# Kernel optimization log

Measured on AMD Instinct MI355X. Metric: run time of the kernel, lower is better.

## Reference

```python
import jax, jax.numpy as jnp
import numpy as np

EPS = 1e-5
NB, NP, NA, NROT = 16, 1024, 12, 60
C0, C1 = 64, 128
CIN, CFEAT, COUT = 256, 512, 256


def _bn(x, g, b):
    # training-mode BatchNorm1d: stats over batch (+ spatial) dims, channel dim 1
    axes = (0,) if x.ndim == 2 else (0, 2)
    m = x.mean(axis=axes, keepdims=True)
    v = x.var(axis=axes, keepdims=True)
    sh = [1] * x.ndim; sh[1] = -1
    return (x - m) * jax.lax.rsqrt(v + EPS) * g.reshape(sh) + b.reshape(sh)


def _hat(v):  # (n,3) -> (n,3,3) skew-symmetric
    z = jnp.zeros_like(v[:, 0])
    return jnp.stack([z, -v[:, 2], v[:, 1],
                      v[:, 2], z, -v[:, 0],
                      -v[:, 1], v[:, 0], z], axis=-1).reshape(-1, 3, 3)


def _exp_so3(v):  # Rodrigues formula, (n,3) -> (n,3,3)
    theta = jnp.linalg.norm(v, axis=-1, keepdims=True)  # (n,1)
    k = v / jnp.where(theta < 1e-8, 1.0, theta)
    K = _hat(k)
    s = jnp.sin(theta)[..., None]
    c = (1.0 - jnp.cos(theta))[..., None]
    I = jnp.eye(3, dtype=v.dtype)
    return I + s * K + c * (K @ K)


def _pointnet(xyz, feats, W, b, g, bb):
    # PointnetSO3Conv: concat xyz (expanded over anchors) with feats, 1x1 conv, max over points
    nb, _, npts, na = feats.shape
    x = jnp.concatenate([jnp.broadcast_to(xyz[:, :, :, None], (nb, 3, npts, na)), feats], axis=1)
    y = jnp.einsum('oc,bcpa->bopa', W, x) + b[None, :, None, None]
    y = y.max(axis=2)  # max over points -> (nb, o, na)
    return jax.nn.relu(_bn(y, g, bb))


def setup_inputs() -> dict:
    key = jax.random.key(0)
    ks = iter(jax.random.split(key, 64))
    def nrm(shape, s=0.1):
        return jax.random.normal(next(ks), shape, dtype=jnp.float32) * s
    d = {
        'xyz0': nrm((NB, 3, NP), 1.0),
        'feats0': nrm((NB, C0, NP, NA), 1.0),
        'xyz1': nrm((NB, 3, NP), 1.0),
        'feats1': nrm((NB, C1, NP, NA), 1.0),
        'trace_idx': jax.random.randint(next(ks), (NA, NROT), 0, NA),
        'anchors': nrm((NROT, 3, 3), 1.0),
        'pn0_W': nrm((C0, C0 + 3)), 'pn0_b': nrm((C0,)), 'pn0_g': jnp.ones((C0,), jnp.float32), 'pn0_bb': jnp.zeros((C0,), jnp.float32),
        'pn1_W': nrm((C1, C1 + 3)), 'pn1_b': nrm((C1,)), 'pn1_g': jnp.ones((C1,), jnp.float32), 'pn1_bb': jnp.zeros((C1,), jnp.float32),
        'lin_W': nrm((CIN, C0 + C1)), 'lin_b': nrm((CIN,)), 'lin_g': jnp.ones((CIN,), jnp.float32), 'lin_bb': jnp.zeros((CIN,), jnp.float32),
        'feat_W': nrm((CFEAT, CIN * NA)), 'feat_b': nrm((CFEAT,)), 'feat_g': jnp.ones((CFEAT,), jnp.float32), 'feat_bb': jnp.zeros((CFEAT,), jnp.float32),
        'att_W1': nrm((128, CFEAT)), 'att_b1': nrm((128,)), 'att_g': jnp.ones((128,), jnp.float32), 'att_bb': jnp.zeros((128,), jnp.float32),
        'att_W2': nrm((1, 128)), 'att_b2': nrm((1,)),
        'reg_W1': nrm((128, CFEAT)), 'reg_b1': nrm((128,)), 'reg_g': jnp.ones((128,), jnp.float32), 'reg_bb': jnp.zeros((128,), jnp.float32),
        'reg_W2': nrm((7, 128)), 'reg_b2': nrm((7,)),
        'out_W1': nrm((CFEAT, CFEAT)), 'out_b1': nrm((CFEAT,)), 'out_g': jnp.ones((CFEAT,), jnp.float32), 'out_bb': jnp.zeros((CFEAT,), jnp.float32),
        'out_W2': nrm((COUT, CFEAT)), 'out_b2': nrm((COUT,)),
    }
    return d


def reference(xyz0, feats0, xyz1, feats1, trace_idx, anchors,
              pn0_W, pn0_b, pn0_g, pn0_bb, pn1_W, pn1_b, pn1_g, pn1_bb,
              lin_W, lin_b, lin_g, lin_bb, feat_W, feat_b, feat_g, feat_bb,
              att_W1, att_b1, att_g, att_bb, att_W2, att_b2,
              reg_W1, reg_b1, reg_g, reg_bb, reg_W2, reg_b2,
              out_W1, out_b1, out_g, out_bb, out_W2, out_b2):
    nb = feats0.shape[0]
    # _pooling: per-level pointnet + BN + relu, concat, pn_linear + pn_bn
    p0 = _pointnet(xyz0, feats0, pn0_W, pn0_b, pn0_g, pn0_bb)
    p1 = _pointnet(xyz1, feats1, pn1_W, pn1_b, pn1_g, pn1_bb)
    x = jnp.concatenate([p0, p1], axis=1)                                   # (nb, 192, na)
    x = _bn(jnp.einsum('oc,bca->boa', lin_W, x) + lin_b[None, :, None], lin_g, lin_bb)  # (nb,256,na)
    # gather trace_idx_ori and flatten channel x anchor dims
    x = x[:, :, trace_idx].reshape(nb, CIN * NA, NROT)                      # (nb,3072,60)
    xf = jax.nn.relu(_bn(jnp.einsum('oc,bca->boa', feat_W, x) + feat_b[None, :, None], feat_g, feat_bb))  # (nb,512,60)
    h = jax.nn.relu(_bn(jnp.einsum('oc,bca->boa', reg_W1, xf) + reg_b1[None, :, None], reg_g, reg_bb))
    residual = (jnp.einsum('oc,bca->boa', reg_W2, h) + reg_b2[None, :, None]).transpose(0, 2, 1)  # (nb,60,7)
    res_D = residual[:, :, :3] / jnp.linalg.norm(residual[:, :, :3], axis=-1, keepdims=True)
    res_N = (jax.nn.sigmoid(residual[:, :, 3]) - 0.5) * jnp.pi / 5
    res_V = res_D * res_N[..., None]
    res_R = _exp_so3(res_V.reshape(-1, 3)).reshape(nb, NROT, 3, 3)
    res_T = residual[:, :, 4:]
    pred_R = jnp.einsum('tij,btjk->btik', anchors, res_R)
    # attention head + softmax over 60 rotations
    a = jax.nn.relu(_bn(jnp.einsum('oc,bca->boa', att_W1, xf) + att_b1[None, :, None], att_g, att_bb))
    logits = (jnp.einsum('oc,bca->boa', att_W2, a) + att_b2[None, :, None])[:, 0]   # (nb,60)
    x_attn = jax.nn.softmax(logits, axis=-1)
    # max-pool over rotations + out MLP
    xm = xf.max(axis=-1)                                                    # (nb,512)
    o = jax.nn.relu(_bn(xm @ out_W1.T + out_b1, out_g, out_bb))
    x_out = o @ out_W2.T + out_b2
    return (x_out, x_attn, pred_R, res_T)
```

## Files before the change

### kernel.cpp

```cpp
#include <hip/hip_runtime.h>
#include <math.h>

#define NBATCH 16
#define NPTS   1024
#define NANG   12
#define NROTS  60
#define EPSV   1e-5f

#define WB0_OFF   0
#define WB1_OFF   3072
#define PART0_OFF 13312
#define PART1_OFF 799744
#define FEATW_OFF 13312
#define XF_OFF    13312
#define XM_OFF    504832
#define OACT_OFF  513024
#define XCAT_OFF  2372608
#define XLIN_OFF  2409472
#define XG_OFF    2458624
#define BRP_OFF   2458624
#define HACT_OFF  4424704
#define AACT_OFF  4547584
#define FRAW_OFF  5407744

#define OUT_XOUT 0
#define OUT_ATTN 4096
#define OUT_PRED 5056
#define OUT_REST 13696

typedef short  bf16x8 __attribute__((ext_vector_type(8)));
typedef float  f32x4  __attribute__((ext_vector_type(4)));

__device__ __forceinline__ unsigned short f2bf_rne(float x){
  unsigned int u = __float_as_uint(x);
  u += 0x7FFFu + ((u >> 16) & 1u);
  return (unsigned short)(u >> 16);
}
__device__ __forceinline__ float bf2f(unsigned short h){
  return __uint_as_float(((unsigned int)h) << 16);
}

__device__ __forceinline__ bf16x8 pack8(const float* f){
  union { unsigned int u[4]; bf16x8 v; } r;
  #pragma unroll
  for (int i = 0; i < 4; i++)
    r.u[i] = __builtin_amdgcn_perm(__float_as_uint(f[2*i+1]),
                                   __float_as_uint(f[2*i]), 0x07060302u);
  return r.v;
}

__device__ __forceinline__ void stage16(const unsigned short* g, unsigned short* l){
  __builtin_amdgcn_global_load_lds((const __attribute__((address_space(1))) void*)g,
                                   (__attribute__((address_space(3))) void*)l, 16, 0, 0);
}

template<int NT>
__device__ __forceinline__ void block_stats(float v, float& m, float& var, float* sbuf){
  constexpr int NW = NT / 64;
  float s = v, s2 = v * v;
  #pragma unroll
  for (int off = 32; off; off >>= 1){
    s  += __shfl_xor(s,  off, 64);
    s2 += __shfl_xor(s2, off, 64);
  }
  const int w = threadIdx.x >> 6;
  if ((threadIdx.x & 63) == 0){ sbuf[w] = s; sbuf[NW + w] = s2; }
  __syncthreads();
  float ts = 0.f, ts2 = 0.f;
  #pragma unroll
  for (int i = 0; i < NW; i++){ ts += sbuf[i]; ts2 += sbuf[NW + i]; }
  m = ts / (float)NT;
  var = ts2 / (float)NT - m * m;
}

template<int C>
__global__ void prep_wb(const float* __restrict__ W, unsigned short* __restrict__ Wb){
  constexpr int KPAD = C + 32;
  const int idx = blockIdx.x * 256 + threadIdx.x;
  if (idx >= C * KPAD) return;
  const int o = idx / KPAD, k = idx % KPAD;
  float v = 0.f;
  if (k < C)          v = W[(size_t)o * (C + 3) + 3 + k];
  else if (k < C + 3) v = W[(size_t)o * (C + 3) + (k - C)];
  Wb[idx] = f2bf_rne(v);
}

template<int C>
__global__ __launch_bounds__(256) void pn_mfma(
    const float* __restrict__ xyz, const float* __restrict__ feats,
    const unsigned short* __restrict__ Wb, float* __restrict__ part){
  constexpr int KPAD = C + 32;
  constexpr int NFK  = C / 32;
  constexpr int MT   = C / 16;
  constexpr int SROW = 196;
  const int nchunk = blockIdx.x, b = blockIdx.y;
  const int tid  = threadIdx.x;
  const int lane = tid & 63, wave = tid >> 6;
  const int g = lane >> 4, l16 = lane & 15;
  const int colbase = wave * 48;
  const int nbase   = nchunk * 192;

  __shared__ float Bs[2][32 * SROW];

  int nn[3], pp[3];
  #pragma unroll
  for (int t = 0; t < 3; t++){
    nn[t] = colbase + t * 16 + l16;
    pp[t] = (nbase + nn[t]) / 12;
  }

  f32x4 acc[MT][3];
  #pragma unroll
  for (int m = 0; m < MT; m++)
    #pragma unroll
    for (int t = 0; t < 3; t++)
      acc[m][t] = (f32x4){0.f, 0.f, 0.f, 0.f};

  const float* fB = feats + (size_t)b * C * (NPTS * NANG) + nbase;

  int srow[6], scol[6], sslot[6];
  #pragma unroll
  for (int jj = 0; jj < 6; jj++){
    const int idx = tid + 256 * jj;
    srow[jj]  = idx / 48;
    scol[jj]  = (idx % 48) * 4;
    sslot[jj] = (srow[jj] & 7) * 4 + (srow[jj] >> 3);
  }

  {
    float4 v[6];
    #pragma unroll
    for (int jj = 0; jj < 6; jj++)
      v[jj] = *(const float4*)(fB + (size_t)srow[jj] * (NPTS * NANG) + scol[jj]);
    #pragma unroll
    for (int jj = 0; jj < 6; jj++)
      *(float4*)(&Bs[0][sslot[jj] * SROW + scol[jj]]) = v[jj];
  }
  __syncthreads();

  #pragma unroll
  for (int ks = 0; ks < NFK; ks++){
    const int buf = ks & 1;
    float4 v[6];
    if (ks + 1 < NFK){
      const int kb = (ks + 1) * 32;
      #pragma unroll
      for (int jj = 0; jj < 6; jj++)
        v[jj] = *(const float4*)(fB + (size_t)(kb + srow[jj]) * (NPTS * NANG) + scol[jj]);
    }
    const int kb = ks * 32;
    bf16x8 Bf[3];
    #pragma unroll
    for (int t = 0; t < 3; t++){
      float f[8];
      #pragma unroll
      for (int j = 0; j < 8; j++)
        f[j] = Bs[buf][(j * 4 + g) * SROW + nn[t]];
      Bf[t] = pack8(f);
    }
    #pragma unroll
    for (int m = 0; m < MT; m++){
      const bf16x8 Af = *(const bf16x8*)(Wb + (size_t)(m * 16 + l16) * KPAD + kb + g * 8);
      #pragma unroll
      for (int t = 0; t < 3; t++)
        acc[m][t] = __builtin_amdgcn_mfma_f32_16x16x32_bf16(Af, Bf[t], acc[m][t], 0, 0, 0);
    }
    if (ks + 1 < NFK){
      #pragma unroll
      for (int jj = 0; jj < 6; jj++)
        *(float4*)(&Bs[buf ^ 1][sslot[jj] * SROW + scol[jj]]) = v[jj];
    }
    __syncthreads();
  }

  {
    const int kb = C;
    bf16x8 Bf[3];
    #pragma unroll
    for (int t = 0; t < 3; t++){
      float f[8];
      #pragma unroll
      for (int j = 0; j < 8; j++) f[j] = 0.f;
      if (g == 0){
        #pragma unroll
        for (int j = 0; j < 3; j++)
          f[j] = xyz[(size_t)(b * 3 + j) * NPTS + pp[t]];
      }
      Bf[t] = pack8(f);
    }
    #pragma unroll
    for (int m = 0; m < MT; m++){
      const bf16x8 Af = *(const bf16x8*)(Wb + (size_t)(m * 16 + l16) * KPAD + kb + g * 8);
      #pragma unroll
      for (int t = 0; t < 3; t++)
        acc[m][t] = __builtin_amdgcn_mfma_f32_16x16x32_bf16(Af, Bf[t], acc[m][t], 0, 0, 0);
    }
  }

  float* yb = &Bs[0][0];
  #pragma unroll
  for (int m = 0; m < MT; m++){
    __syncthreads();
    #pragma unroll
    for (int t = 0; t < 3; t++)
      #pragma unroll
      for (int r = 0; r < 4; r++)
        yb[(g * 4 + r) * SROW + nn[t]] = acc[m][t][r];
    __syncthreads();
    if (tid < 192){
      const int o_l = tid / 12, a = tid % 12;
      float mx = -3.4e38f;
      #pragma unroll
      for (int pl = 0; pl < 16; pl++)
        mx = fmaxf(mx, yb[o_l * SROW + pl * 12 + a]);
      part[((size_t)(b * 64 + nchunk) * C + m * 16 + o_l) * 12 + a] = mx;
    }
  }
}

__global__ void pn_reduce_bn(const float* __restrict__ part0, const float* __restrict__ part1,
    const float* __restrict__ b0, const float* __restrict__ g0, const float* __restrict__ bb0,
    const float* __restrict__ b1, const float* __restrict__ g1, const float* __restrict__ bb1,
    float* __restrict__ xcat){
  const int ch = blockIdx.x, t = threadIdx.x;
  const int b = t / 12, a = t % 12;
  const float* part; const float *bias, *g, *bb; int o, Cl;
  if (ch < 64){ part = part0; bias = b0; g = g0; bb = bb0; o = ch;      Cl = 64;  }
  else        { part = part1; bias = b1; g = g1; bb = bb1; o = ch - 64; Cl = 128; }
  const float* pp = part + ((size_t)(b * 64) * Cl + o) * 12 + a;
  const size_t kstride = (size_t)Cl * 12;
  float v = pp[0];
  for (int k = 1; k < 64; k++) v = fmaxf(v, pp[(size_t)k * kstride]);
  v += bias[o];
  __shared__ float sbuf[8];
  float m, var;
  block_stats<192>(v, m, var, sbuf);
  float xn = (v - m) * rsqrtf(var + EPSV) * g[o] + bb[o];
  xcat[((size_t)b * 192 + ch) * 12 + a] = fmaxf(xn, 0.f);
}

__global__ void lin_bn(const float* __restrict__ xcat, const float* __restrict__ W,
    const float* __restrict__ bias, const float* __restrict__ g, const float* __restrict__ bb,
    float* __restrict__ xlin){
  const int o = blockIdx.x, t = threadIdx.x;
  const int b = t / 12, a = t % 12;
  const float* xr = xcat + (size_t)b * 2304 + a;
  const float* wr = W + (size_t)o * 192;
  float v = bias[o];
  for (int c = 0; c < 192; c++) v = fmaf(wr[c], xr[(size_t)c * 12], v);
  __shared__ float sbuf[8];
  float m, var;
  block_stats<192>(v, m, var, sbuf);
  xlin[((size_t)b * 256 + o) * 12 + a] = (v - m) * rsqrtf(var + EPSV) * g[o] + bb[o];
}

__global__ void prep_featw(const float* __restrict__ W, unsigned short* __restrict__ Wb2){
  const int idx = blockIdx.x * 256 + threadIdx.x;
  if (idx >= 512 * 3072) return;
  const int o = idx / 3072, k = idx % 3072;
  const float x = W[idx];
  const unsigned short hi = f2bf_rne(x);
  const unsigned short lo = f2bf_rne(x - bf2f(hi));
  Wb2[(size_t)o * 6144 + k] = hi;
  Wb2[(size_t)o * 6144 + 3072 + k] = lo;
}

__global__ void prep_xg(const float* __restrict__ xlin, const int* __restrict__ trace,
                        unsigned short* __restrict__ Xg){
  const int n = blockIdx.x;
  const int b = n / 60, r = n % 60;
  unsigned short* row = Xg + (size_t)n * 6144;
  __shared__ int ta[12];
  if (threadIdx.x < 12) ta[threadIdx.x] = trace[threadIdx.x * 60 + r];
  __syncthreads();
  for (int i = threadIdx.x; i < 3072; i += 256){
    const int c = i / 12, a = i % 12;
    const float x = xlin[((size_t)b * 256 + c) * 12 + ta[a]];
    const unsigned short hi = f2bf_rne(x);
    const unsigned short lo = f2bf_rne(x - bf2f(hi));
    row[i] = hi;
    row[3072 + i] = lo;
  }
}

__global__ __launch_bounds__(256) void feat_mfma(
    const unsigned short* __restrict__ Wb2, const unsigned short* __restrict__ Xg,
    float* __restrict__ fraw){
  const int nblk = blockIdx.x, mblk = blockIdx.y, seg = blockIdx.z;
  const int tid = threadIdx.x;
  const int lane = tid & 63, wave = tid >> 6;
  const int g = lane >> 4, l16 = lane & 15;
  const int kA = (seg == 1) ? 3072 : 0;
  const int kB = (seg == 2) ? 3072 : 0;
  const int sw = l16 & 7;
  const int wm = wave >> 1, wn = wave & 1;

  __shared__ unsigned short As[2][64 * 64];
  __shared__ unsigned short Bs[2][64 * 64];

  int rowj[2], colj[2], ldsoff[2];
  #pragma unroll
  for (int j = 0; j < 2; j++){
    const int idx = j * 256 + wave * 64 + lane;
    rowj[j]   = idx >> 3;
    colj[j]   = ((idx & 7) ^ (rowj[j] & 7)) * 8;
    ldsoff[j] = (j * 256 + wave * 64) * 8;
  }
  const unsigned short* Agb = Wb2 + (size_t)mblk * 64 * 6144 + kA;
  const unsigned short* Bgb = Xg  + (size_t)nblk * 64 * 6144 + kB;

  f32x4 acc[2][2];
  #pragma unroll
  for (int i = 0; i < 2; i++)
    #pragma unroll
    for (int j = 0; j < 2; j++)
      acc[i][j] = (f32x4){0.f, 0.f, 0.f, 0.f};

  #pragma unroll
  for (int j = 0; j < 2; j++){
    stage16(Agb + (size_t)rowj[j] * 6144 + colj[j], &As[0][ldsoff[j]]);
    stage16(Bgb + (size_t)rowj[j] * 6144 + colj[j], &Bs[0][ldsoff[j]]);
  }
  __syncthreads();

  for (int kc = 0; kc < 3072; kc += 64){
    const int buf = (kc >> 6) & 1;
    if (kc + 64 < 3072){
      const int kn = kc + 64;
      #pragma unroll
      for (int j = 0; j < 2; j++){
        stage16(Agb + (size_t)rowj[j] * 6144 + kn + colj[j], &As[buf ^ 1][ldsoff[j]]);
        stage16(Bgb + (size_t)rowj[j] * 6144 + kn + colj[j], &Bs[buf ^ 1][ldsoff[j]]);
      }
    }
    #pragma unroll
    for (int kc2 = 0; kc2 < 64; kc2 += 32){
      const int c0 = kc2 >> 3;
      bf16x8 af[2], bfr[2];
      #pragma unroll
      for (int i = 0; i < 2; i++)
        af[i]  = *(const bf16x8*)&As[buf][(wm * 32 + i * 16 + l16) * 64 + ((c0 + g) ^ sw) * 8];
      #pragma unroll
      for (int i = 0; i < 2; i++)
        bfr[i] = *(const bf16x8*)&Bs[buf][(wn * 32 + i * 16 + l16) * 64 + ((c0 + g) ^ sw) * 8];
      #pragma unroll
      for (int i = 0; i < 2; i++)
        #pragma unroll
        for (int j = 0; j < 2; j++)
          acc[i][j] = __builtin_amdgcn_mfma_f32_16x16x32_bf16(af[i], bfr[j], acc[i][j], 0, 0, 0);
    }
    __syncthreads();
  }

  float* base = fraw + (size_t)seg * (512 * 960);
  #pragma unroll
  for (int i = 0; i < 2; i++)
    #pragma unroll
    for (int j = 0; j < 2; j++){
      const int n = nblk * 64 + wn * 32 + j * 16 + l16;
      #pragma unroll
      for (int q = 0; q < 4; q++){
        const int m = mblk * 64 + wm * 32 + i * 16 + g * 4 + q;
        base[(size_t)m * 960 + n] = acc[i][j][q];
      }
    }
}

__global__ void feat_bn(const float* __restrict__ fraw, const float* __restrict__ bias,
    const float* __restrict__ g, const float* __restrict__ bb,
    float* __restrict__ xf, float* __restrict__ xm){
  const int o = blockIdx.x, t = threadIdx.x;
  const int b = t / 60, r = t % 60;
  const size_t SS = (size_t)512 * 960;
  const size_t in = (size_t)o * 960 + t;
  float v = fraw[in] + fraw[SS + in] + fraw[2 * SS + in] + bias[o];
  __shared__ float sbuf[32];
  float m, var;
  block_stats<960>(v, m, var, sbuf);
  const float xn = fmaxf((v - m) * rsqrtf(var + EPSV) * g[o] + bb[o], 0.f);
  xf[((size_t)b * 512 + o) * 60 + r] = xn;
  __shared__ float red[960];
  red[t] = xn;
  __syncthreads();
  if (r == 0){
    float mx = red[t];
    for (int k = 1; k < 60; k++) mx = fmaxf(mx, red[t + k]);
    xm[(size_t)b * 512 + o] = mx;
  }
}

__global__ __launch_bounds__(256) void brgemm2(const float* __restrict__ xf,
    const float* __restrict__ Wr, const float* __restrict__ Wa,
    float* __restrict__ brp){
  const int og = blockIdx.x, b = blockIdx.y, z = blockIdx.z;
  const int br = z >> 3, ks = z & 7;
  const float* W = br ? Wa : Wr;
  const int lane = threadIdx.x & 63, wave = threadIdx.x >> 6;
  const int obase = og * 32 + wave * 8;
  const int rr = lane < 60 ? lane : 0;
  const float* xb = xf + ((size_t)b * 512 + ks * 64) * 60 + rr;
  const float* wr = W + (size_t)obase * 512 + ks * 64;

  float acc[8];
  #pragma unroll
  for (int i = 0; i < 8; i++) acc[i] = 0.f;

  float cur[4], nxt[4];
  #pragma unroll
  for (int j = 0; j < 4; j++) cur[j] = xb[(size_t)j * 60];

  for (int c0 = 0; c0 < 64; c0 += 4){
    #pragma unroll
    for (int j = 0; j < 4; j++){
      int cc = c0 + 4 + j; if (cc > 63) cc = 63;
      nxt[j] = xb[(size_t)cc * 60];
    }
    #pragma unroll
    for (int j = 0; j < 4; j++)
      #pragma unroll
      for (int i = 0; i < 8; i++)
        acc[i] = fmaf(wr[(size_t)i * 512 + c0 + j], cur[j], acc[i]);
    #pragma unroll
    for (int j = 0; j < 4; j++) cur[j] = nxt[j];
  }

  if (lane < 60){
    #pragma unroll
    for (int i = 0; i < 8; i++)
      brp[(((size_t)z * NBATCH + b) * 128 + obase + i) * 60 + lane] = acc[i];
  }
}

__global__ void br_bn(const float* __restrict__ brp,
    const float* __restrict__ biasR, const float* __restrict__ gR, const float* __restrict__ bbR,
    const float* __restrict__ biasA, const float* __restrict__ gA, const float* __restrict__ bbA,
    float* __restrict__ hact, float* __restrict__ aact){
  const int o = blockIdx.x, br = blockIdx.y, t = threadIdx.x;
  const int b = t / 60, r = t % 60;
  const float* bias = br ? biasA : biasR;
  const float* g    = br ? gA    : gR;
  const float* bb   = br ? bbA   : bbR;
  float v = bias[o];
  #pragma unroll
  for (int ks = 0; ks < 8; ks++)
    v += brp[((((size_t)br * 8 + ks) * NBATCH + b) * 128 + o) * 60 + r];
  __shared__ float sbuf[32];
  float m, var;
  block_stats<960>(v, m, var, sbuf);
  float* outp = br ? aact : hact;
  outp[((size_t)b * 128 + o) * 60 + r] =
      fmaxf((v - m) * rsqrtf(var + EPSV) * g[o] + bb[o], 0.f);
}

__global__ void reg2_geom(const float* __restrict__ h, const float* __restrict__ W2,
    const float* __restrict__ b2, const float* __restrict__ anchors, float* __restrict__ out){
  const int b = blockIdx.x, lane = threadIdx.x;
  const int r = lane < 60 ? lane : 59;
  float res[7];
  #pragma unroll
  for (int j = 0; j < 7; j++){
    float acc = b2[j];
    for (int c = 0; c < 128; c++)
      acc = fmaf(W2[j * 128 + c], h[((size_t)b * 128 + c) * 60 + r], acc);
    res[j] = acc;
  }
  if (lane >= 60) return;
  const float n = sqrtf(res[0]*res[0] + res[1]*res[1] + res[2]*res[2]);
  const float invn = 1.f / n;
  const float Nv = (1.f / (1.f + expf(-res[3])) - 0.5f) * 3.14159265358979323846f / 5.f;
  const float v0 = res[0]*invn*Nv, v1 = res[1]*invn*Nv, v2 = res[2]*invn*Nv;
  const float th = sqrtf(v0*v0 + v1*v1 + v2*v2);
  const float invt = th < 1e-8f ? 1.f : 1.f / th;
  const float k0 = v0*invt, k1 = v1*invt, k2 = v2*invt;
  const float s = sinf(th), cc = 1.f - cosf(th);
  const float K[9] = {0.f, -k2, k1,  k2, 0.f, -k0,  -k1, k0, 0.f};
  float K2[9];
  #pragma unroll
  for (int ii = 0; ii < 3; ii++)
    #pragma unroll
    for (int jj = 0; jj < 3; jj++)
      K2[ii*3+jj] = K[ii*3+0]*K[0*3+jj] + K[ii*3+1]*K[1*3+jj] + K[ii*3+2]*K[2*3+jj];
  float R[9];
  #pragma unroll
  for (int ii = 0; ii < 3; ii++)
    #pragma unroll
    for (int jj = 0; jj < 3; jj++)
      R[ii*3+jj] = (ii == jj ? 1.f : 0.f) + s * K[ii*3+jj] + cc * K2[ii*3+jj];
  const float* A = anchors + (size_t)r * 9;
  #pragma unroll
  for (int ii = 0; ii < 3; ii++)
    #pragma unroll
    for (int kk = 0; kk < 3; kk++){
      const float pv = A[ii*3+0]*R[0*3+kk] + A[ii*3+1]*R[1*3+kk] + A[ii*3+2]*R[2*3+kk];
      out[OUT_PRED + ((size_t)b * 60 + r) * 9 + ii * 3 + kk] = pv;
    }
  #pragma unroll
  for (int k = 0; k < 3; k++)
    out[OUT_REST + ((size_t)b * 60 + r) * 3 + k] = res[4 + k];
}

__global__ void att2_softmax(const float* __restrict__ a, const float* __restrict__ W2,
    const float* __restrict__ b2, float* __restrict__ out){
  const int b = blockIdx.x, lane = threadIdx.x;
  const int r = lane < 60 ? lane : 59;
  float acc = b2[0];
  for (int c = 0; c < 128; c++)
    acc = fmaf(W2[c], a[((size_t)b * 128 + c) * 60 + r], acc);
  const float l = lane < 60 ? acc : -INFINITY;
  float mx = l;
  #pragma unroll
  for (int off = 32; off; off >>= 1) mx = fmaxf(mx, __shfl_xor(mx, off, 64));
  const float e = lane < 60 ? expf(l - mx) : 0.f;
  float ssum = e;
  #pragma unroll
  for (int off = 32; off; off >>= 1) ssum += __shfl_xor(ssum, off, 64);
  if (lane < 60) out[OUT_ATTN + (size_t)b * 60 + lane] = e / ssum;
}

__global__ void out_head1(const float* __restrict__ xm, const float* __restrict__ W1,
    const float* __restrict__ b1, const float* __restrict__ g, const float* __restrict__ bb,
    float* __restrict__ o_act){
  const int t = threadIdx.x;
  const int b = t & 15, j = t >> 4;
  const int oc = blockIdx.x * 8 + j;
  float acc = b1[oc];
  const float* wr = W1 + (size_t)oc * 512;
  const float* xr = xm + (size_t)b * 512;
  for (int c = 0; c < 512; c++) acc = fmaf(wr[c], xr[c], acc);
  float s = acc, s2 = acc * acc;
  #pragma unroll
  for (int off = 8; off; off >>= 1){
    s  += __shfl_xor(s,  off, 16);
    s2 += __shfl_xor(s2, off, 16);
  }
  const float m = s * (1.f / 16.f);
  const float var = s2 * (1.f / 16.f) - m * m;
  o_act[(size_t)b * 512 + oc] = fmaxf((acc - m) * rsqrtf(var + EPSV) * g[oc] + bb[oc], 0.f);
}

__global__ void out_head2(const float* __restrict__ o_act, const float* __restrict__ W2,
    const float* __restrict__ b2, float* __restrict__ out){
  const int b = blockIdx.x, j = threadIdx.x;
  const float* wr = W2 + (size_t)j * 512;
  const float* xr = o_act + (size_t)b * 512;
  float acc = b2[j];
  for (int c = 0; c < 512; c++) acc = fmaf(wr[c], xr[c], acc);
  out[OUT_XOUT + (size_t)b * 256 + j] = acc;
}

extern "C" void kernel_launch(void* const* d_in, const int* in_sizes, int n_in,
                              void* d_out, int out_size, void* d_ws, size_t ws_size,
                              hipStream_t stream){
  const float* xyz0    = (const float*)d_in[0];
  const float* feats0  = (const float*)d_in[1];
  const float* xyz1    = (const float*)d_in[2];
  const float* feats1  = (const float*)d_in[3];
  const int*   trace   = (const int*)  d_in[4];
  const float* anchors = (const float*)d_in[5];
  const float* pn0_W  = (const float*)d_in[6];
  const float* pn0_b  = (const float*)d_in[7];
  const float* pn0_g  = (const float*)d_in[8];
  const float* pn0_bb = (const float*)d_in[9];
  const float* pn1_W  = (const float*)d_in[10];
  const float* pn1_b  = (const float*)d_in[11];
  const float* pn1_g  = (const float*)d_in[12];
  const float* pn1_bb = (const float*)d_in[13];
  const float* lin_W  = (const float*)d_in[14];
  const float* lin_b  = (const float*)d_in[15];
  const float* lin_g  = (const float*)d_in[16];
  const float* lin_bb = (const float*)d_in[17];
  const float* feat_W  = (const float*)d_in[18];
  const float* feat_b  = (const float*)d_in[19];
  const float* feat_g  = (const float*)d_in[20];
  const float* feat_bb = (const float*)d_in[21];
  const float* att_W1 = (const float*)d_in[22];
  const float* att_b1 = (const float*)d_in[23];
  const float* att_g  = (const float*)d_in[24];
  const float* att_bb = (const float*)d_in[25];
  const float* att_W2 = (const float*)d_in[26];
  const float* att_b2 = (const float*)d_in[27];
  const float* reg_W1 = (const float*)d_in[28];
  const float* reg_b1 = (const float*)d_in[29];
  const float* reg_g  = (const float*)d_in[30];
  const float* reg_bb = (const float*)d_in[31];
  const float* reg_W2 = (const float*)d_in[32];
  const float* reg_b2 = (const float*)d_in[33];
  const float* out_W1 = (const float*)d_in[34];
  const float* out_b1 = (const float*)d_in[35];
  const float* out_g  = (const float*)d_in[36];
  const float* out_bb = (const float*)d_in[37];
  const float* out_W2 = (const float*)d_in[38];
  const float* out_b2 = (const float*)d_in[39];

  float* ws  = (float*)d_ws;
  float* out = (float*)d_out;
  unsigned short* wb0 = (unsigned short*)(ws + WB0_OFF);
  unsigned short* wb1 = (unsigned short*)(ws + WB1_OFF);
  unsigned short* fw  = (unsigned short*)(ws + FEATW_OFF);
  unsigned short* xg  = (unsigned short*)(ws + XG_OFF);

  prep_wb<64> <<<24, 256, 0, stream>>>(pn0_W, wb0);
  prep_wb<128><<<80, 256, 0, stream>>>(pn1_W, wb1);

  pn_mfma<64> <<<dim3(64, 16), 256, 0, stream>>>(xyz0, feats0, wb0, ws + PART0_OFF);
  pn_mfma<128><<<dim3(64, 16), 256, 0, stream>>>(xyz1, feats1, wb1, ws + PART1_OFF);

  pn_reduce_bn<<<192, 192, 0, stream>>>(ws + PART0_OFF, ws + PART1_OFF,
      pn0_b, pn0_g, pn0_bb, pn1_b, pn1_g, pn1_bb, ws + XCAT_OFF);

  prep_featw<<<6144, 256, 0, stream>>>(feat_W, fw);

  lin_bn<<<256, 192, 0, stream>>>(ws + XCAT_OFF, lin_W, lin_b, lin_g, lin_bb, ws + XLIN_OFF);

  prep_xg<<<960, 256, 0, stream>>>(ws + XLIN_OFF, trace, xg);

  feat_mfma<<<dim3(15, 8, 3), 256, 0, stream>>>(fw, xg, ws + FRAW_OFF);
  feat_bn<<<512, 960, 0, stream>>>(ws + FRAW_OFF, feat_b, feat_g, feat_bb,
                                   ws + XF_OFF, ws + XM_OFF);

  brgemm2<<<dim3(4, 16, 16), 256, 0, stream>>>(ws + XF_OFF, reg_W1, att_W1, ws + BRP_OFF);
  br_bn<<<dim3(128, 2), 960, 0, stream>>>(ws + BRP_OFF,
      reg_b1, reg_g, reg_bb, att_b1, att_g, att_bb,
      ws + HACT_OFF, ws + AACT_OFF);

  reg2_geom<<<16, 64, 0, stream>>>(ws + HACT_OFF, reg_W2, reg_b2, anchors, out);
  att2_softmax<<<16, 64, 0, stream>>>(ws + AACT_OFF, att_W2, att_b2, out);
  out_head1<<<64, 128, 0, stream>>>(ws + XM_OFF, out_W1, out_b1, out_g, out_bb, ws + OACT_OFF);
  out_head2<<<16, 256, 0, stream>>>(ws + OACT_OFF, out_W2, out_b2, out);
}
```

Before: 485.9 us.

## Merge independent kernels to cut launch count and run pointnet branches concurrently

Result: faster. 431.1 us (-11.3%).

```diff
diff --git a/kernel.cpp b/kernel.cpp
--- a/kernel.cpp
+++ b/kernel.cpp
@@ -11,7 +11,6 @@
 #define WB1_OFF   3072
 #define PART0_OFF 13312
 #define PART1_OFF 799744
-#define FEATW_OFF 13312
 #define XF_OFF    13312
 #define XM_OFF    504832
 #define OACT_OFF  513024
@@ -22,6 +21,7 @@
 #define HACT_OFF  4424704
 #define AACT_OFF  4547584
 #define FRAW_OFF  5407744
+#define FEATW_OFF 6882304
 
 #define OUT_XOUT 0
 #define OUT_ATTN 4096
@@ -74,9 +74,9 @@
 }
 
 template<int C>
-__global__ void prep_wb(const float* __restrict__ W, unsigned short* __restrict__ Wb){
+__device__ __forceinline__ void prep_wb_body(int idx, const float* __restrict__ W,
+                                             unsigned short* __restrict__ Wb){
   constexpr int KPAD = C + 32;
-  const int idx = blockIdx.x * 256 + threadIdx.x;
   if (idx >= C * KPAD) return;
   const int o = idx / KPAD, k = idx % KPAD;
   float v = 0.f;
@@ -85,14 +85,36 @@
   Wb[idx] = f2bf_rne(v);
 }
 
+__global__ __launch_bounds__(256) void prep_all(
+    const float* __restrict__ W0, const float* __restrict__ W1,
+    const float* __restrict__ FW,
+    unsigned short* __restrict__ wb0, unsigned short* __restrict__ wb1,
+    unsigned short* __restrict__ fw2){
+  const int blk = blockIdx.x;
+  if (blk < 24){
+    prep_wb_body<64>(blk * 256 + threadIdx.x, W0, wb0);
+  } else if (blk < 104){
+    prep_wb_body<128>((blk - 24) * 256 + threadIdx.x, W1, wb1);
+  } else {
+    const int idx = (blk - 104) * 256 + threadIdx.x;
+    const int o = idx / 3072, k = idx % 3072;
+    const float x = FW[idx];
+    const unsigned short hi = f2bf_rne(x);
+    const unsigned short lo = f2bf_rne(x - bf2f(hi));
+    fw2[(size_t)o * 6144 + k] = hi;
+    fw2[(size_t)o * 6144 + 3072 + k] = lo;
+  }
+}
+
+#define SROW 196
 template<int C>
-__global__ __launch_bounds__(256) void pn_mfma(
+__device__ __forceinline__ void pn_body(
     const float* __restrict__ xyz, const float* __restrict__ feats,
-    const unsigned short* __restrict__ Wb, float* __restrict__ part){
+    const unsigned short* __restrict__ Wb, float* __restrict__ part,
+    float* Bs ){
   constexpr int KPAD = C + 32;
   constexpr int NFK  = C / 32;
   constexpr int MT   = C / 16;
-  constexpr int SROW = 196;
   const int nchunk = blockIdx.x, b = blockIdx.y;
   const int tid  = threadIdx.x;
   const int lane = tid & 63, wave = tid >> 6;
@@ -100,8 +122,6 @@
   const int colbase = wave * 48;
   const int nbase   = nchunk * 192;
 
-  __shared__ float Bs[2][32 * SROW];
-
   int nn[3], pp[3];
   #pragma unroll
   for (int t = 0; t < 3; t++){
@@ -134,13 +154,14 @@
       v[jj] = *(const float4*)(fB + (size_t)srow[jj] * (NPTS * NANG) + scol[jj]);
     #pragma unroll
     for (int jj = 0; jj < 6; jj++)
-      *(float4*)(&Bs[0][sslot[jj] * SROW + scol[jj]]) = v[jj];
+      *(float4*)(&Bs[sslot[jj] * SROW + scol[jj]]) = v[jj];
   }
   __syncthreads();
 
   #pragma unroll
   for (int ks = 0; ks < NFK; ks++){
-    const int buf = ks & 1;
+    float* Bc = Bs + (ks & 1) * (32 * SROW);
+    float* Bn = Bs + ((ks & 1) ^ 1) * (32 * SROW);
     float4 v[6];
     if (ks + 1 < NFK){
       const int kb = (ks + 1) * 32;
@@ -155,7 +176,7 @@
       float f[8];
       #pragma unroll
       for (int j = 0; j < 8; j++)
-        f[j] = Bs[buf][(j * 4 + g) * SROW + nn[t]];
+        f[j] = Bc[(j * 4 + g) * SROW + nn[t]];
       Bf[t] = pack8(f);
     }
     #pragma unroll
@@ -168,7 +189,7 @@
     if (ks + 1 < NFK){
       #pragma unroll
       for (int jj = 0; jj < 6; jj++)
-        *(float4*)(&Bs[buf ^ 1][sslot[jj] * SROW + scol[jj]]) = v[jj];
+        *(float4*)(&Bn[sslot[jj] * SROW + scol[jj]]) = v[jj];
     }
     __syncthreads();
   }
@@ -197,7 +218,7 @@
     }
   }
 
-  float* yb = &Bs[0][0];
+  float* yb = Bs;
   #pragma unroll
   for (int m = 0; m < MT; m++){
     __syncthreads();
@@ -216,6 +237,16 @@
       part[((size_t)(b * 64 + nchunk) * C + m * 16 + o_l) * 12 + a] = mx;
     }
   }
+}
+
+__global__ __launch_bounds__(256) void pn_both(
+    const float* __restrict__ xyz0, const float* __restrict__ feats0,
+    const unsigned short* __restrict__ wb0, float* __restrict__ part0,
+    const float* __restrict__ xyz1, const float* __restrict__ feats1,
+    const unsigned short* __restrict__ wb1, float* __restrict__ part1){
+  __shared__ float Bs[2 * 32 * SROW];
+  if (blockIdx.z == 0) pn_body<64> (xyz0, feats0, wb0, part0, Bs);
+  else                 pn_body<128>(xyz1, feats1, wb1, part1, Bs);
 }
 
 __global__ void pn_reduce_bn(const float* __restrict__ part0, const float* __restrict__ part1,
@@ -252,17 +283,6 @@
   float m, var;
   block_stats<192>(v, m, var, sbuf);
   xlin[((size_t)b * 256 + o) * 12 + a] = (v - m) * rsqrtf(var + EPSV) * g[o] + bb[o];
-}
-
-__global__ void prep_featw(const float* __restrict__ W, unsigned short* __restrict__ Wb2){
-  const int idx = blockIdx.x * 256 + threadIdx.x;
-  if (idx >= 512 * 3072) return;
-  const int o = idx / 3072, k = idx % 3072;
-  const float x = W[idx];
-  const unsigned short hi = f2bf_rne(x);
-  const unsigned short lo = f2bf_rne(x - bf2f(hi));
-  Wb2[(size_t)o * 6144 + k] = hi;
-  Wb2[(size_t)o * 6144 + 3072 + k] = lo;
 }
 
 __global__ void prep_xg(const float* __restrict__ xlin, const int* __restrict__ trace,
@@ -389,14 +409,39 @@
   }
 }
 
-__global__ __launch_bounds__(256) void brgemm2(const float* __restrict__ xf,
+__global__ __launch_bounds__(256) void brgemm_oh1(const float* __restrict__ xf,
     const float* __restrict__ Wr, const float* __restrict__ Wa,
-    float* __restrict__ brp){
-  const int og = blockIdx.x, b = blockIdx.y, z = blockIdx.z;
+    float* __restrict__ brp,
+    const float* __restrict__ xm, const float* __restrict__ oW1,
+    const float* __restrict__ ob1, const float* __restrict__ og,
+    const float* __restrict__ obb, float* __restrict__ o_act){
+  const int z = blockIdx.z;
+  if (z == 16){
+    const int q = blockIdx.y * 4 + blockIdx.x;
+    if (q >= 32) return;
+    const int t = threadIdx.x;
+    const int b = t & 15, j = t >> 4;
+    const int oc = q * 16 + j;
+    float acc = ob1[oc];
+    const float* wr = oW1 + (size_t)oc * 512;
+    const float* xr = xm + (size_t)b * 512;
+    for (int c = 0; c < 512; c++) acc = fmaf(wr[c], xr[c], acc);
+    float s = acc, s2 = acc * acc;
+    #pragma unroll
+    for (int off = 8; off; off >>= 1){
+      s  += __shfl_xor(s,  off, 16);
+      s2 += __shfl_xor(s2, off, 16);
+    }
+    const float m = s * (1.f / 16.f);
+    const float var = s2 * (1.f / 16.f) - m * m;
+    o_act[(size_t)b * 512 + oc] = fmaxf((acc - m) * rsqrtf(var + EPSV) * og[oc] + obb[oc], 0.f);
+    return;
+  }
+  const int og_ = blockIdx.x, b = blockIdx.y;
   const int br = z >> 3, ks = z & 7;
   const float* W = br ? Wa : Wr;
   const int lane = threadIdx.x & 63, wave = threadIdx.x >> 6;
-  const int obase = og * 32 + wave * 8;
+  const int obase = og_ * 32 + wave * 8;
   const int rr = lane < 60 ? lane : 0;
   const float* xb = xf + ((size_t)b * 512 + ks * 64) * 60 + rr;
   const float* wr = W + (size_t)obase * 512 + ks * 64;
@@ -452,100 +497,79 @@
       fmaxf((v - m) * rsqrtf(var + EPSV) * g[o] + bb[o], 0.f);
 }
 
-__global__ void reg2_geom(const float* __restrict__ h, const float* __restrict__ W2,
-    const float* __restrict__ b2, const float* __restrict__ anchors, float* __restrict__ out){
-  const int b = blockIdx.x, lane = threadIdx.x;
-  const int r = lane < 60 ? lane : 59;
-  float res[7];
-  #pragma unroll
-  for (int j = 0; j < 7; j++){
-    float acc = b2[j];
+__global__ void heads(
+    const float* __restrict__ h, const float* __restrict__ rW2,
+    const float* __restrict__ rb2, const float* __restrict__ anchors,
+    const float* __restrict__ a, const float* __restrict__ aW2, const float* __restrict__ ab2,
+    const float* __restrict__ o_act, const float* __restrict__ oW2,
+    const float* __restrict__ ob2, float* __restrict__ out){
+  const int b = blockIdx.x, sel = blockIdx.y, t = threadIdx.x;
+  if (sel == 0){
+    if (t >= 64) return;
+    const int r = t < 60 ? t : 59;
+    float res[7];
+    #pragma unroll
+    for (int j = 0; j < 7; j++) res[j] = rb2[j];
+    for (int c = 0; c < 128; c++){
+      const float hv = h[((size_t)b * 128 + c) * 60 + r];
+      #pragma unroll
+      for (int j = 0; j < 7; j++) res[j] = fmaf(rW2[j * 128 + c], hv, res[j]);
+    }
+    if (t >= 60) return;
+    const float n = sqrtf(res[0]*res[0] + res[1]*res[1] + res[2]*res[2]);
+    const float invn = 1.f / n;
+    const float Nv = (1.f / (1.f + expf(-res[3])) - 0.5f) * 3.14159265358979323846f / 5.f;
+    const float v0 = res[0]*invn*Nv, v1 = res[1]*invn*Nv, v2 = res[2]*invn*Nv;
+    const float th = sqrtf(v0*v0 + v1*v1 + v2*v2);
+    const float invt = th < 1e-8f ? 1.f : 1.f / th;
+    const float k0 = v0*invt, k1 = v1*invt, k2 = v2*invt;
+    const float s = sinf(th), cc = 1.f - cosf(th);
+    const float K[9] = {0.f, -k2, k1,  k2, 0.f, -k0,  -k1, k0, 0.f};
+    float K2[9];
+    #pragma unroll
+    for (int ii = 0; ii < 3; ii++)
+      #pragma unroll
+      for (int jj = 0; jj < 3; jj++)
+        K2[ii*3+jj] = K[ii*3+0]*K[0*3+jj] + K[ii*3+1]*K[1*3+jj] + K[ii*3+2]*K[2*3+jj];
+    float R[9];
+    #pragma unroll
+    for (int ii = 0; ii < 3; ii++)
+      #pragma unroll
+      for (int jj = 0; jj < 3; jj++)
+        R[ii*3+jj] = (ii == jj ? 1.f : 0.f) + s * K[ii*3+jj] + cc * K2[ii*3+jj];
+    const float* A = anchors + (size_t)t * 9;
+    #pragma unroll
+    for (int ii = 0; ii < 3; ii++)
+      #pragma unroll
+      for (int kk = 0; kk < 3; kk++){
+        const float pv = A[ii*3+0]*R[0*3+kk] + A[ii*3+1]*R[1*3+kk] + A[ii*3+2]*R[2*3+kk];
+        out[OUT_PRED + ((size_t)b * 60 + t) * 9 + ii * 3 + kk] = pv;
+      }
+    #pragma unroll
+    for (int k = 0; k < 3; k++)
+      out[OUT_REST + ((size_t)b * 60 + t) * 3 + k] = res[4 + k];
+  } else if (sel == 1){
+    if (t >= 64) return;
+    const int r = t < 60 ? t : 59;
+    float acc = ab2[0];
     for (int c = 0; c < 128; c++)
-      acc = fmaf(W2[j * 128 + c], h[((size_t)b * 128 + c) * 60 + r], acc);
-    res[j] = acc;
-  }
-  if (lane >= 60) return;
-  const float n = sqrtf(res[0]*res[0] + res[1]*res[1] + res[2]*res[2]);
-  const float invn = 1.f / n;
-  const float Nv = (1.f / (1.f + expf(-res[3])) - 0.5f) * 3.14159265358979323846f / 5.f;
-  const float v0 = res[0]*invn*Nv, v1 = res[1]*invn*Nv, v2 = res[2]*invn*Nv;
-  const float th = sqrtf(v0*v0 + v1*v1 + v2*v2);
-  const float invt = th < 1e-8f ? 1.f : 1.f / th;
-  const float k0 = v0*invt, k1 = v1*invt, k2 = v2*invt;
-  const float s = sinf(th), cc = 1.f - cosf(th);
-  const float K[9] = {0.f, -k2, k1,  k2, 0.f, -k0,  -k1, k0, 0.f};
-  float K2[9];
-  #pragma unroll
-  for (int ii = 0; ii < 3; ii++)
-    #pragma unroll
-    for (int jj = 0; jj < 3; jj++)
-      K2[ii*3+jj] = K[ii*3+0]*K[0*3+jj] + K[ii*3+1]*K[1*3+jj] + K[ii*3+2]*K[2*3+jj];
-  float R[9];
-  #pragma unroll
-  for (int ii = 0; ii < 3; ii++)
-    #pragma unroll
-    for (int jj = 0; jj < 3; jj++)
-      R[ii*3+jj] = (ii == jj ? 1.f : 0.f) + s * K[ii*3+jj] + cc * K2[ii*3+jj];
-  const float* A = anchors + (size_t)r * 9;
-  #pragma unroll
-  for (int ii = 0; ii < 3; ii++)
-    #pragma unroll
-    for (int kk = 0; kk < 3; kk++){
-      const float pv = A[ii*3+0]*R[0*3+kk] + A[ii*3+1]*R[1*3+kk] + A[ii*3+2]*R[2*3+kk];
-      out[OUT_PRED + ((size_t)b * 60 + r) * 9 + ii * 3 + kk] = pv;
-    }
-  #pragma unroll
-  for (int k = 0; k < 3; k++)
-    out[OUT_REST + ((size_t)b * 60 + r) * 3 + k] = res[4 + k];
-}
-
-__global__ void att2_softmax(const float* __restrict__ a, const float* __restrict__ W2,
-    const float* __restrict__ b2, float* __restrict__ out){
-  const int b = blockIdx.x, lane = threadIdx.x;
-  const int r = lane < 60 ? lane : 59;
-  float acc = b2[0];
-  for (int c = 0; c < 128; c++)
-    acc = fmaf(W2[c], a[((size_t)b * 128 + c) * 60 + r], acc);
-  const float l = lane < 60 ? acc : -INFINITY;
-  float mx = l;
-  #pragma unroll
-  for (int off = 32; off; off >>= 1) mx = fmaxf(mx, __shfl_xor(mx, off, 64));
-  const float e = lane < 60 ? expf(l - mx) : 0.f;
-  float ssum = e;
-  #pragma unroll
-  for (int off = 32; off; off >>= 1) ssum += __shfl_xor(ssum, off, 64);
-  if (lane < 60) out[OUT_ATTN + (size_t)b * 60 + lane] = e / ssum;
-}
-
-__global__ void out_head1(const float* __restrict__ xm, const float* __restrict__ W1,
-    const float* __restrict__ b1, const float* __restrict__ g, const float* __restrict__ bb,
-    float* __restrict__ o_act){
-  const int t = threadIdx.x;
-  const int b = t & 15, j = t >> 4;
-  const int oc = blockIdx.x * 8 + j;
-  float acc = b1[oc];
-  const float* wr = W1 + (size_t)oc * 512;
-  const float* xr = xm + (size_t)b * 512;
-  for (int c = 0; c < 512; c++) acc = fmaf(wr[c], xr[c], acc);
-  float s = acc, s2 = acc * acc;
-  #pragma unroll
-  for (int off = 8; off; off >>= 1){
-    s  += __shfl_xor(s,  off, 16);
-    s2 += __shfl_xor(s2, off, 16);
-  }
-  const float m = s * (1.f / 16.f);
-  const float var = s2 * (1.f / 16.f) - m * m;
-  o_act[(size_t)b * 512 + oc] = fmaxf((acc - m) * rsqrtf(var + EPSV) * g[oc] + bb[oc], 0.f);
-}
-
-__global__ void out_head2(const float* __restrict__ o_act, const float* __restrict__ W2,
-    const float* __restrict__ b2, float* __restrict__ out){
-  const int b = blockIdx.x, j = threadIdx.x;
-  const float* wr = W2 + (size_t)j * 512;
-  const float* xr = o_act + (size_t)b * 512;
-  float acc = b2[j];
-  for (int c = 0; c < 512; c++) acc = fmaf(wr[c], xr[c], acc);
-  out[OUT_XOUT + (size_t)b * 256 + j] = acc;
+      acc = fmaf(aW2[c], a[((size_t)b * 128 + c) * 60 + r], acc);
+    const float l = t < 60 ? acc : -INFINITY;
+    float mx = l;
+    #pragma unroll
+    for (int off = 32; off; off >>= 1) mx = fmaxf(mx, __shfl_xor(mx, off, 64));
+    const float e = t < 60 ? expf(l - mx) : 0.f;
+    float ssum = e;
+    #pragma unroll
+    for (int off = 32; off; off >>= 1) ssum += __shfl_xor(ssum, off, 64);
+    if (t < 60) out[OUT_ATTN + (size_t)b * 60 + t] = e / ssum;
+  } else {
+    const float* wr = oW2 + (size_t)t * 512;
+    const float* xr = o_act + (size_t)b * 512;
+    float acc = ob2[t];
+    for (int c = 0; c < 512; c++) acc = fmaf(wr[c], xr[c], acc);
+    out[OUT_XOUT + (size_t)b * 256 + t] = acc;
+  }
 }
 
 extern "C" void kernel_launch(void* const* d_in, const int* in_sizes, int n_in,
@@ -599,32 +623,30 @@
   unsigned short* fw  = (unsigned short*)(ws + FEATW_OFF);
   unsigned short* xg  = (unsigned short*)(ws + XG_OFF);
 
-  prep_wb<64> <<<24, 256, 0, stream>>>(pn0_W, wb0);
-  prep_wb<128><<<80, 256, 0, stream>>>(pn1_W, wb1);
-
-  pn_mfma<64> <<<dim3(64, 16), 256, 0, stream>>>(xyz0, feats0, wb0, ws + PART0_OFF);
-  pn_mfma<128><<<dim3(64, 16), 256, 0, stream>>>(xyz1, feats1, wb1, ws + PART1_OFF);
+  prep_all<<<6248, 256, 0, stream>>>(pn0_W, pn1_W, feat_W, wb0, wb1, fw);
+
+  pn_both<<<dim3(64, 16, 2), 256, 0, stream>>>(xyz0, feats0, wb0, ws + PART0_OFF,
+                                               xyz1, feats1, wb1, ws + PART1_OFF);
 
   pn_reduce_bn<<<192, 192, 0, stream>>>(ws + PART0_OFF, ws + PART1_OFF,
       pn0_b, pn0_g, pn0_bb, pn1_b, pn1_g, pn1_bb, ws + XCAT_OFF);
 
-  prep_featw<<<6144, 256, 0, stream>>>(feat_W, fw);
-
   lin_bn<<<256, 192, 0, stream>>>(ws + XCAT_OFF, lin_W, lin_b, lin_g, lin_bb, ws + XLIN_OFF);
 
   prep_xg<<<960, 256, 0, stream>>>(ws + XLIN_OFF, trace, xg);
 
   feat_mfma<<<dim3(15, 8, 3), 256, 0, stream>>>(fw, xg, ws + FRAW_OFF);
+
   feat_bn<<<512, 960, 0, stream>>>(ws + FRAW_OFF, feat_b, feat_g, feat_bb,
                                    ws + XF_OFF, ws + XM_OFF);
 
-  brgemm2<<<dim3(4, 16, 16), 256, 0, stream>>>(ws + XF_OFF, reg_W1, att_W1, ws + BRP_OFF);
+  brgemm_oh1<<<dim3(4, 16, 17), 256, 0, stream>>>(ws + XF_OFF, reg_W1, att_W1, ws + BRP_OFF,
+      ws + XM_OFF, out_W1, out_b1, out_g, out_bb, ws + OACT_OFF);
+
   br_bn<<<dim3(128, 2), 960, 0, stream>>>(ws + BRP_OFF,
       reg_b1, reg_g, reg_bb, att_b1, att_g, att_bb,
       ws + HACT_OFF, ws + AACT_OFF);
 
-  reg2_geom<<<16, 64, 0, stream>>>(ws + HACT_OFF, reg_W2, reg_b2, anchors, out);
-  att2_softmax<<<16, 64, 0, stream>>>(ws + AACT_OFF, att_W2, att_b2, out);
-  out_head1<<<64, 128, 0, stream>>>(ws + XM_OFF, out_W1, out_b1, out_g, out_bb, ws + OACT_OFF);
-  out_head2<<<16, 256, 0, stream>>>(ws + OACT_OFF, out_W2, out_b2, out);
-}
+  heads<<<dim3(16, 3), 256, 0, stream>>>(ws + HACT_OFF, reg_W2, reg_b2, anchors,
+      ws + AACT_OFF, att_W2, att_b2, ws + OACT_OFF, out_W2, out_b2, out);
+}
```
